# Kernel tuning notes

Hardware: AMD Instinct MI355X
Metric: run time of the kernel (lower is better)

## Reference

```python
import jax, jax.numpy as jnp
import numpy as np

# Hypernetwork config (matches init_kwargs)
INP = 4096      # inp_size
MSK = 64        # mask_size
HID = 64        # node_hidden_size (target-net hidden)
OUT = 10        # out_size (target outputs)
L1, L2, L3 = 64, 256, 128  # hypernet trunk layers
B = 16384       # batch
WVEC = MSK * HID + HID + HID * OUT + OUT  # 4810 generated weights per sample


def _linear_params(key, fan_in, fan_out):
    # torch.nn.Linear default init: U(-1/sqrt(fan_in), 1/sqrt(fan_in))
    lim = 1.0 / np.sqrt(fan_in)
    kw, kb = jax.random.split(key)
    W = jax.random.uniform(kw, (fan_out, fan_in), minval=-lim, maxval=lim, dtype=jnp.float32)
    b = jax.random.uniform(kb, (fan_out,), minval=-lim, maxval=lim, dtype=jnp.float32)
    return W, b


def setup_inputs() -> dict:
    key = jax.random.key(0)
    ks = jax.random.split(key, 6)
    W1, b1 = _linear_params(ks[0], INP, L1)
    W2, b2 = _linear_params(ks[1], L1, L2)
    W3, b3 = _linear_params(ks[2], L2, L3)
    W4, b4 = _linear_params(ks[3], L3, WVEC)
    data = jax.random.normal(ks[4], (B, INP), dtype=jnp.float32)
    mask_idx = jnp.sort(jax.random.randint(ks[5], (B, MSK), 0, INP), axis=1)  # int indices of active features
    return dict(data=data, mask_idx=mask_idx,
                W1=W1, b1=b1, W2=W2, b2=b2, W3=W3, b3=b3, W4=W4, b4=b4)


def reference(data, mask_idx, W1, b1, W2, b2, W3, b3, W4, b4):
    b = data.shape[0]
    # Rebuild the float binary mask [B, INP] from indices (scatter ones)
    rows = jnp.arange(b)[:, None]
    mask = jnp.zeros((b, INP), dtype=data.dtype).at[rows, mask_idx].set(1.0)

    # craft_network: 4-layer MLP on the mask (dropout is identity in eval / for reference)
    h = jax.nn.relu(mask @ W1.T + b1)
    h = jax.nn.relu(h @ W2.T + b2)
    h = jax.nn.relu(h @ W3.T + b3)
    w = h @ W4.T + b4  # [B, WVEC] generated weights per sample

    # Split per-sample generated weights (same layout as InsertableNet)
    iw_end = MSK * HID
    ib_end = iw_end + HID
    ow_end = ib_end + HID * OUT
    inp_w = w[:, :iw_end].reshape(b, HID, MSK)       # [B, H, M]
    inp_b = w[:, iw_end:ib_end]                      # [B, H]
    out_w = w[:, ib_end:ow_end].reshape(b, OUT, HID) # [B, O, H]
    out_b = w[:, ow_end:]                            # [B, O]

    # Per-sample gather of masked features: data[i, mask[i]] -> [B, M]
    xm = jnp.take_along_axis(data, mask_idx, axis=1)

    # Batched tiny 2-layer MLP (replaces the per-sample Python loop)
    hid = jax.nn.relu(jnp.einsum('bhm,bm->bh', inp_w, xm) + inp_b)
    res = jnp.einsum('boh,bh->bo', out_w, hid) + out_b  # [B, OUT]
    return res
```

## Files before the change

kernel.cpp:

```cpp
#include <hip/hip_runtime.h>


typedef _Float16 f16;
typedef _Float16 f16x8 __attribute__((ext_vector_type(8)));
typedef _Float16 f16x4 __attribute__((ext_vector_type(4)));
typedef float    f32x4 __attribute__((ext_vector_type(4)));

#define NPAD 4864

#define BAR() do { asm volatile("s_waitcnt lgkmcnt(0)" ::: "memory"); \
                   __builtin_amdgcn_s_barrier();                      \
                   asm volatile("" ::: "memory"); } while (0)

__global__ __launch_bounds__(256) void k_prep(
    const float* __restrict__ W1, const float* __restrict__ W2,
    const float* __restrict__ W3, const float* __restrict__ W4,
    f16* __restrict__ W1Th, f16* __restrict__ W2h,
    f16* __restrict__ W3h, f16* __restrict__ W4s)
{
    const int tid = blockIdx.x * 256 + threadIdx.x;
    const int stride = gridDim.x * 256;
    for (int e = tid; e < 4096 * 64; e += stride) {
        int j = e >> 6, i = e & 63;
        W1Th[e] = (f16)W1[(size_t)i * 4096 + j];
    }
    for (int e = tid; e < NPAD * 128; e += stride) {
        const int j    = e & 7;
        const int lane = (e >> 3) & 63;
        const int mt   = (e >> 9) & 3;
        const int kk   = (e >> 11) & 3;
        const int c    = e >> 13;
        const int lr = lane & 15, g = lane >> 4;
        const int row = 64 * c + 16 * mt + lr;
        const int col = 32 * kk + 8 * g + j;
        W4s[e] = (row < 4810) ? (f16)W4[(size_t)row * 128 + col] : (f16)0.f;
    }
    for (int e = tid; e < 256 * 64; e += stride)  W2h[e] = (f16)W2[e];
    for (int e = tid; e < 128 * 256; e += stride) W3h[e] = (f16)W3[e];
}

__global__ __launch_bounds__(512, 2) void k_main(
    const float* __restrict__ data, const int* __restrict__ midx,
    const f16* __restrict__ W1Th, const float* __restrict__ b1,
    const f16* __restrict__ W2h, const float* __restrict__ b2,
    const f16* __restrict__ W3h, const float* __restrict__ b3,
    const f16* __restrict__ W4s, const float* __restrict__ b4,
    float* __restrict__ out)
{
    __shared__ __align__(16) int   idx_s[64 * 64];
    __shared__ __align__(16) char  h1b[8192];
    __shared__ __align__(16) char  h2b[32768];
    __shared__ __align__(16) char  h3b[16384];
    __shared__ __align__(16) float xm_s[64 * 68];
    __shared__ __align__(16) float hid_s[64 * 68];
    __shared__ __align__(16) f16   w64_s[64 * 64];
    __shared__ __align__(16) float res_s[64 * 12];
    __shared__ __align__(16) float res_b[64 * 12];

    const int t = threadIdx.x, w = t >> 6, lane = t & 63;
    const int lr = lane & 15, g = lane >> 4;
    const int row0 = blockIdx.x * 64;
    const f32x4 zero = {0.f, 0.f, 0.f, 0.f};

    for (int e = t; e < 4096; e += 512)
        idx_s[e] = midx[(size_t)row0 * 64 + e];
    BAR();

    float xr[64];

    if (w == 7) {
        #pragma unroll
        for (int k = 0; k < 64; ++k)
            xr[k] = data[(size_t)(row0 + k) * 4096 + idx_s[k * 64 + lane]];
        __builtin_amdgcn_sched_barrier(0);
    } else {
        const f32x4 b1v = *(const f32x4*)&b1[lr * 4];
        for (int sp = w; sp < 32; sp += 7) {
            const int s0 = 2 * sp, s1 = s0 + 1;
            f32x4 a0 = zero, a1 = zero;
            #pragma unroll
            for (int tt = 0; tt < 16; ++tt) {
                const int i = g * 16 + tt;
                const int c0 = idx_s[s0 * 64 + i];
                const int q0 = (i > 0) ? idx_s[s0 * 64 + i - 1] : -1;
                const int c1 = idx_s[s1 * 64 + i];
                const int q1 = (i > 0) ? idx_s[s1 * 64 + i - 1] : -1;
                const f16x4 w0 = *(const f16x4*)&W1Th[c0 * 64 + lr * 4];
                const f16x4 w1 = *(const f16x4*)&W1Th[c1 * 64 + lr * 4];
                #pragma unroll
                for (int q = 0; q < 4; ++q) {
                    a0[q] += (c0 != q0) ? (float)w0[q] : 0.f;
                    a1[q] += (c1 != q1) ? (float)w1[q] : 0.f;
                }
            }
            #pragma unroll
            for (int q = 0; q < 4; ++q) {
                a0[q] += __shfl_xor(a0[q], 16);
                a0[q] += __shfl_xor(a0[q], 32);
                a1[q] += __shfl_xor(a1[q], 16);
                a1[q] += __shfl_xor(a1[q], 32);
            }
            if (g == 0) {
                f16x4 h0, h1v;
                #pragma unroll
                for (int q = 0; q < 4; ++q) {
                    h0[q]  = (f16)fmaxf(a0[q] + b1v[q], 0.f);
                    h1v[q] = (f16)fmaxf(a1[q] + b1v[q], 0.f);
                }
                *(f16x4*)(h1b + ((s0 * 128 + lr * 8) ^ ((s0 & 7) << 4))) = h0;
                *(f16x4*)(h1b + ((s1 * 128 + lr * 8) ^ ((s1 & 7) << 4))) = h1v;
            }
        }
    }
    BAR();

    if (w < 7) {
        f16x8 bh[4][2];
        #pragma unroll
        for (int rt = 0; rt < 4; ++rt)
            #pragma unroll
            for (int kk = 0; kk < 2; ++kk) {
                const int s = 16 * rt + lr;
                bh[rt][kk] = *(const f16x8*)(h1b + ((s * 128 + (32 * kk + 8 * g) * 2) ^ ((s & 7) << 4)));
            }
        for (int nb = w; nb < 8; nb += 7) {
            const int n0 = 32 * nb;
            f16x8 a2[2][2];
            #pragma unroll
            for (int mt = 0; mt < 2; ++mt)
                #pragma unroll
                for (int kk = 0; kk < 2; ++kk)
                    a2[mt][kk] = *(const f16x8*)&W2h[(n0 + 16 * mt + lr) * 64 + 32 * kk + 8 * g];
            f32x4 acc2[2][4];
            #pragma unroll
            for (int mt = 0; mt < 2; ++mt)
                #pragma unroll
                for (int rt = 0; rt < 4; ++rt) {
                    acc2[mt][rt] = __builtin_amdgcn_mfma_f32_16x16x32_f16(a2[mt][0], bh[rt][0], zero, 0, 0, 0);
                    acc2[mt][rt] = __builtin_amdgcn_mfma_f32_16x16x32_f16(a2[mt][1], bh[rt][1], acc2[mt][rt], 0, 0, 0);
                }
            #pragma unroll
            for (int mt = 0; mt < 2; ++mt) {
                const f32x4 bv = *(const f32x4*)&b2[n0 + 16 * mt + 4 * g];
                #pragma unroll
                for (int rt = 0; rt < 4; ++rt) {
                    const int s = 16 * rt + lr;
                    f16x4 hv;
                    #pragma unroll
                    for (int q = 0; q < 4; ++q)
                        hv[q] = (f16)fmaxf(acc2[mt][rt][q] + bv[q], 0.f);
                    *(f16x4*)(h2b + ((s * 512 + (n0 + 16 * mt + 4 * g) * 2) ^ ((s & 7) << 4))) = hv;
                }
            }
        }
    }
    BAR();

    if (w < 7) {
        for (int nb = w; nb < 8; nb += 7) {
            const int n0 = 16 * nb;
            f32x4 acc3[4] = {zero, zero, zero, zero};
            #pragma unroll 2
            for (int kk = 0; kk < 8; ++kk) {
                const f16x8 a3 = *(const f16x8*)&W3h[(n0 + lr) * 256 + 32 * kk + 8 * g];
                #pragma unroll
                for (int rt = 0; rt < 4; ++rt) {
                    const int s = 16 * rt + lr;
                    const f16x8 bb = *(const f16x8*)(h2b + ((s * 512 + (32 * kk + 8 * g) * 2) ^ ((s & 7) << 4)));
                    acc3[rt] = __builtin_amdgcn_mfma_f32_16x16x32_f16(a3, bb, acc3[rt], 0, 0, 0);
                }
            }
            const f32x4 bv3 = *(const f32x4*)&b3[n0 + 4 * g];
            #pragma unroll
            for (int rt = 0; rt < 4; ++rt) {
                const int s = 16 * rt + lr;
                f16x4 hv;
                #pragma unroll
                for (int q = 0; q < 4; ++q)
                    hv[q] = (f16)fmaxf(acc3[rt][q] + bv3[q], 0.f);
                *(f16x4*)(h3b + ((s * 256 + (n0 + 4 * g) * 2) ^ ((s & 7) << 4))) = hv;
            }
        }
    }
    BAR();

    f16x8 bfrag[4][4];
    #pragma unroll
    for (int u = 0; u < 4; ++u)
        #pragma unroll
        for (int kk = 0; kk < 4; ++kk) {
            const int s = 16 * u + lr;
            bfrag[kk][u] = *(const f16x8*)(h3b + ((s * 256 + (32 * kk + 8 * g) * 2) ^ ((s & 7) << 4)));
        }
    if (w == 7) {
        #pragma unroll
        for (int k = 0; k < 64; ++k)
            xm_s[k * 68 + lane] = xr[k];
    }
    BAR();

    f16x4 xmr[4][4];
    #pragma unroll
    for (int mt = 0; mt < 4; ++mt)
        #pragma unroll
        for (int u = 0; u < 4; ++u) {
            const f32x4 xv = *(const f32x4*)&xm_s[(16 * u + lr) * 68 + 16 * mt + 4 * g];
            f16x4 xh;
            #pragma unroll
            for (int q = 0; q < 4; ++q) xh[q] = (f16)xv[q];
            xmr[mt][u] = xh;
        }

    const char* W4b = (const char*)W4s;
    const int afoff = lane * 16;

#define LDAF(dst, c, kk) { const char* cb_ = W4b + (size_t)(c) * 16384 + (kk) * 4096 + afoff; \
    dst[0] = *(const f16x8*)(cb_);        dst[1] = *(const f16x8*)(cb_ + 1024); \
    dst[2] = *(const f16x8*)(cb_ + 2048); dst[3] = *(const f16x8*)(cb_ + 3072); }

#define MFMA16(af, kk) { \
    _Pragma("unroll") for (int mt = 0; mt < 4; ++mt) \
    _Pragma("unroll") for (int u = 0; u < 4; ++u) \
        acc[mt][u] = __builtin_amdgcn_mfma_f32_16x16x32_f16(af[mt], bfrag[kk][u], acc[mt][u], 0, 0, 0); }

    for (int c = w; c < 65; c += 8) {
        f16x8 afA[4], afB[4];
        LDAF(afA, c, 0)
        LDAF(afB, c, 1)
        f32x4 acc[4][4];
        #pragma unroll
        for (int mt = 0; mt < 4; ++mt)
            #pragma unroll
            for (int u = 0; u < 4; ++u)
                acc[mt][u] = __builtin_amdgcn_mfma_f32_16x16x32_f16(afA[mt], bfrag[0][u], zero, 0, 0, 0);
        LDAF(afA, c, 2)
        MFMA16(afB, 1)
        LDAF(afB, c, 3)
        MFMA16(afA, 2)
        MFMA16(afB, 3)

        f32x4 bv[4];
        #pragma unroll
        for (int mt = 0; mt < 4; ++mt)
            bv[mt] = *(const f32x4*)&b4[64 * c + 16 * mt + 4 * g];

        if (c < 64) {
            #pragma unroll
            for (int u = 0; u < 4; ++u) {
                float sum = 0.f;
                #pragma unroll
                for (int mt = 0; mt < 4; ++mt)
                    #pragma unroll
                    for (int q = 0; q < 4; ++q)
                        sum += (acc[mt][u][q] + bv[mt][q]) * (float)xmr[mt][u][q];
                sum += __shfl_xor(sum, 16);
                sum += __shfl_xor(sum, 32);
                if (g == 0) hid_s[(16 * u + lr) * 68 + c] = sum;
            }
        } else {
            #pragma unroll
            for (int u = 0; u < 4; ++u)
                #pragma unroll
                for (int mt = 0; mt < 4; ++mt) {
                    f16x4 wv;
                    #pragma unroll
                    for (int q = 0; q < 4; ++q)
                        wv[q] = (f16)(acc[mt][u][q] + bv[mt][q]);
                    *(f16x4*)&w64_s[(16 * u + lr) * 64 + 16 * mt + 4 * g] = wv;
                }
        }
    }
    BAR();

    f16x4 hidr[4][4];
    #pragma unroll
    for (int mt = 0; mt < 4; ++mt)
        #pragma unroll
        for (int u = 0; u < 4; ++u) {
            const int s = 16 * u + lr;
            f16x4 xh;
            #pragma unroll
            for (int q = 0; q < 4; ++q) {
                const int h = 16 * mt + 4 * g + q;
                xh[q] = (f16)fmaxf(hid_s[s * 68 + h] + (float)w64_s[s * 64 + h], 0.f);
            }
            hidr[mt][u] = xh;
        }

    auto do_out = [&](int c) {
        f32x4 bv[4];
        #pragma unroll
        for (int mt = 0; mt < 4; ++mt)
            bv[mt] = *(const f32x4*)&b4[64 * c + 16 * mt + 4 * g];
        f16x8 afA[4], afB[4];
        LDAF(afA, c, 0)
        LDAF(afB, c, 1)
        f32x4 acc[4][4];
        #pragma unroll
        for (int mt = 0; mt < 4; ++mt)
            #pragma unroll
            for (int u = 0; u < 4; ++u)
                acc[mt][u] = __builtin_amdgcn_mfma_f32_16x16x32_f16(afA[mt], bfrag[0][u], zero, 0, 0, 0);
        LDAF(afA, c, 2)
        MFMA16(afB, 1)
        LDAF(afB, c, 3)
        MFMA16(afA, 2)
        MFMA16(afB, 3)
        #pragma unroll
        for (int u = 0; u < 4; ++u) {
            float sum = 0.f;
            #pragma unroll
            for (int mt = 0; mt < 4; ++mt)
                #pragma unroll
                for (int q = 0; q < 4; ++q)
                    sum += (acc[mt][u][q] + bv[mt][q]) * (float)hidr[mt][u][q];
            sum += __shfl_xor(sum, 16);
            sum += __shfl_xor(sum, 32);
            if (g == 0) res_s[(16 * u + lr) * 12 + (c - 65)] = sum;
        }
    };
    do_out(65 + w);
    if (w < 2) do_out(73 + w);

    if (w == 2) {
        f32x4 accb[4] = {zero, zero, zero, zero};
        #pragma unroll
        for (int kk = 0; kk < 4; ++kk) {
            const f16x8 af = *(const f16x8*)(W4b + (size_t)75 * 16384 + kk * 4096 + afoff);
            #pragma unroll
            for (int u = 0; u < 4; ++u)
                accb[u] = __builtin_amdgcn_mfma_f32_16x16x32_f16(af, bfrag[kk][u], accb[u], 0, 0, 0);
        }
        #pragma unroll
        for (int u = 0; u < 4; ++u)
            #pragma unroll
            for (int q = 0; q < 4; ++q) {
                const int o = 4 * g + q;
                if (o < 10)
                    res_b[(16 * u + lr) * 12 + o] = accb[u][q] + b4[4800 + o];
            }
    }
    BAR();

    for (int e = t; e < 640; e += 512)
        out[(size_t)row0 * 10 + e] =
            res_s[(e / 10) * 12 + (e % 10)] + res_b[(e / 10) * 12 + (e % 10)];
#undef LDAF
#undef MFMA16
}

extern "C" void kernel_launch(void* const* d_in, const int* in_sizes, int n_in,
                              void* d_out, int out_size, void* d_ws, size_t ws_size,
                              hipStream_t stream)
{
    const float* data = (const float*)d_in[0];
    const int*   midx = (const int*)d_in[1];
    const float* W1   = (const float*)d_in[2];
    const float* b1   = (const float*)d_in[3];
    const float* W2   = (const float*)d_in[4];
    const float* b2   = (const float*)d_in[5];
    const float* W3   = (const float*)d_in[6];
    const float* b3   = (const float*)d_in[7];
    const float* W4   = (const float*)d_in[8];
    const float* b4   = (const float*)d_in[9];
    float* out = (float*)d_out;

    f16* W1Th = (f16*)d_ws;
    f16* W4s  = W1Th + (size_t)4096 * 64;
    f16* W2h  = W4s + (size_t)NPAD * 128;
    f16* W3h  = W2h + 256 * 64;

    k_prep<<<512, 256, 0, stream>>>(W1, W2, W3, W4, W1Th, W2h, W3h, W4s);
    k_main<<<256, 512, 0, stream>>>(data, midx, W1Th, b1, W2h, b2, W3h, b3,
                                    W4s, b4, out);
}
```

Before: 74.89 us.

## Split gather across two waves and tile W1 transpose through shared memory

In the main kernel, the per-sample data gather moves from one wave handling 64 rows to two waves handling 32 rows each. This halves the register array each gathering wave holds and spreads the gather latency across two waves. In exchange, only six waves remain for the layer-1/2/3 compute, so each compute wave takes on more iterations. The prep kernel also transposes W1 through a padded shared-memory tile, giving coalesced reads and writes in place of strided reads, though it assumes the grid has more than 64 blocks.

```diff
diff --git a/kernel.cpp b/kernel.cpp
--- a/kernel.cpp
+++ b/kernel.cpp
@@ -18,12 +18,28 @@
     f16* __restrict__ W1Th, f16* __restrict__ W2h,
     f16* __restrict__ W3h, f16* __restrict__ W4s)
 {
-    const int tid = blockIdx.x * 256 + threadIdx.x;
-    const int stride = gridDim.x * 256;
-    for (int e = tid; e < 4096 * 64; e += stride) {
-        int j = e >> 6, i = e & 63;
-        W1Th[e] = (f16)W1[(size_t)i * 4096 + j];
-    }
+    const int bid = blockIdx.x;
+    const int t = threadIdx.x;
+
+    if (bid < 64) {
+        __shared__ float tile[64][65];
+        const int r4 = t >> 6, c0 = t & 63;
+        #pragma unroll
+        for (int rr = 0; rr < 16; ++rr) {
+            const int i = rr * 4 + r4;
+            tile[i][c0] = W1[(size_t)i * 4096 + bid * 64 + c0];
+        }
+        __syncthreads();
+        #pragma unroll
+        for (int rr = 0; rr < 16; ++rr) {
+            const int jj = rr * 4 + r4;
+            W1Th[(size_t)(bid * 64 + jj) * 64 + c0] = (f16)tile[c0][jj];
+        }
+        return;
+    }
+
+    const int tid = (bid - 64) * 256 + t;
+    const int stride = (gridDim.x - 64) * 256;
     for (int e = tid; e < NPAD * 128; e += stride) {
         const int j    = e & 7;
         const int lane = (e >> 3) & 63;
@@ -66,16 +82,17 @@
         idx_s[e] = midx[(size_t)row0 * 64 + e];
     BAR();
 
-    float xr[64];
-
-    if (w == 7) {
-        #pragma unroll
-        for (int k = 0; k < 64; ++k)
-            xr[k] = data[(size_t)(row0 + k) * 4096 + idx_s[k * 64 + lane]];
+    float xr[32];
+
+    if (w >= 6) {
+        const int base = (w - 6) * 32;
+        #pragma unroll
+        for (int k = 0; k < 32; ++k)
+            xr[k] = data[(size_t)(row0 + base + k) * 4096 + idx_s[(base + k) * 64 + lane]];
         __builtin_amdgcn_sched_barrier(0);
     } else {
         const f32x4 b1v = *(const f32x4*)&b1[lr * 4];
-        for (int sp = w; sp < 32; sp += 7) {
+        for (int sp = w; sp < 32; sp += 6) {
             const int s0 = 2 * sp, s1 = s0 + 1;
             f32x4 a0 = zero, a1 = zero;
             #pragma unroll
@@ -114,7 +131,7 @@
     }
     BAR();
 
-    if (w < 7) {
+    if (w < 6) {
         f16x8 bh[4][2];
         #pragma unroll
         for (int rt = 0; rt < 4; ++rt)
@@ -123,7 +140,7 @@
                 const int s = 16 * rt + lr;
                 bh[rt][kk] = *(const f16x8*)(h1b + ((s * 128 + (32 * kk + 8 * g) * 2) ^ ((s & 7) << 4)));
             }
-        for (int nb = w; nb < 8; nb += 7) {
+        for (int nb = w; nb < 8; nb += 6) {
             const int n0 = 32 * nb;
             f16x8 a2[2][2];
             #pragma unroll
@@ -156,8 +173,8 @@
     }
     BAR();
 
-    if (w < 7) {
-        for (int nb = w; nb < 8; nb += 7) {
+    if (w < 6) {
+        for (int nb = w; nb < 8; nb += 6) {
             const int n0 = 16 * nb;
             f32x4 acc3[4] = {zero, zero, zero, zero};
             #pragma unroll 2
@@ -192,10 +209,11 @@
             const int s = 16 * u + lr;
             bfrag[kk][u] = *(const f16x8*)(h3b + ((s * 256 + (32 * kk + 8 * g) * 2) ^ ((s & 7) << 4)));
         }
-    if (w == 7) {
-        #pragma unroll
-        for (int k = 0; k < 64; ++k)
-            xm_s[k * 68 + lane] = xr[k];
+    if (w >= 6) {
+        const int base = (w - 6) * 32;
+        #pragma unroll
+        for (int k = 0; k < 32; ++k)
+            xm_s[(base + k) * 68 + lane] = xr[k];
     }
     BAR();
 
```

Measured after the change: 75.26 us. About the same (+0.5%).

## Fuse weight-prep into main kernel with grid-wide atomic barrier

Applied to the files above, without the earlier changes.

Merges the separate weight conversion kernel into the main kernel. Each block's gather wave loads its data rows while the other waves convert weights: the first 64 blocks transpose W1 through shared memory, and the rest convert W4, W2 and W3. A global atomic counter then acts as a grid barrier before the compute phase. This removes one kernel launch and its serialization and overlaps weight prep with the gather, but it relies on all 256 blocks being co-resident and adds a memset plus spin-wait cost.

```diff
diff --git a/kernel.cpp b/kernel.cpp
--- a/kernel.cpp
+++ b/kernel.cpp
@@ -12,39 +12,15 @@
                    __builtin_amdgcn_s_barrier();                      \
                    asm volatile("" ::: "memory"); } while (0)
 
-__global__ __launch_bounds__(256) void k_prep(
-    const float* __restrict__ W1, const float* __restrict__ W2,
-    const float* __restrict__ W3, const float* __restrict__ W4,
+__global__ __launch_bounds__(512, 2) void k_all(
+    const float* __restrict__ data, const int* __restrict__ midx,
+    const float* __restrict__ W1, const float* __restrict__ b1,
+    const float* __restrict__ W2, const float* __restrict__ b2,
+    const float* __restrict__ W3, const float* __restrict__ b3,
+    const float* __restrict__ W4, const float* __restrict__ b4,
     f16* __restrict__ W1Th, f16* __restrict__ W2h,
-    f16* __restrict__ W3h, f16* __restrict__ W4s)
-{
-    const int tid = blockIdx.x * 256 + threadIdx.x;
-    const int stride = gridDim.x * 256;
-    for (int e = tid; e < 4096 * 64; e += stride) {
-        int j = e >> 6, i = e & 63;
-        W1Th[e] = (f16)W1[(size_t)i * 4096 + j];
-    }
-    for (int e = tid; e < NPAD * 128; e += stride) {
-        const int j    = e & 7;
-        const int lane = (e >> 3) & 63;
-        const int mt   = (e >> 9) & 3;
-        const int kk   = (e >> 11) & 3;
-        const int c    = e >> 13;
-        const int lr = lane & 15, g = lane >> 4;
-        const int row = 64 * c + 16 * mt + lr;
-        const int col = 32 * kk + 8 * g + j;
-        W4s[e] = (row < 4810) ? (f16)W4[(size_t)row * 128 + col] : (f16)0.f;
-    }
-    for (int e = tid; e < 256 * 64; e += stride)  W2h[e] = (f16)W2[e];
-    for (int e = tid; e < 128 * 256; e += stride) W3h[e] = (f16)W3[e];
-}
-
-__global__ __launch_bounds__(512, 2) void k_main(
-    const float* __restrict__ data, const int* __restrict__ midx,
-    const f16* __restrict__ W1Th, const float* __restrict__ b1,
-    const f16* __restrict__ W2h, const float* __restrict__ b2,
-    const f16* __restrict__ W3h, const float* __restrict__ b3,
-    const f16* __restrict__ W4s, const float* __restrict__ b4,
+    f16* __restrict__ W3h, f16* __restrict__ W4s,
+    int* __restrict__ sync_cnt,
     float* __restrict__ out)
 {
     __shared__ __align__(16) int   idx_s[64 * 64];
@@ -59,7 +35,8 @@
 
     const int t = threadIdx.x, w = t >> 6, lane = t & 63;
     const int lr = lane & 15, g = lane >> 4;
-    const int row0 = blockIdx.x * 64;
+    const int bid = blockIdx.x;
+    const int row0 = bid * 64;
     const f32x4 zero = {0.f, 0.f, 0.f, 0.f};
 
     for (int e = t; e < 4096; e += 512)
@@ -74,6 +51,61 @@
             xr[k] = data[(size_t)(row0 + k) * 4096 + idx_s[k * 64 + lane]];
         __builtin_amdgcn_sched_barrier(0);
     } else {
+        if (bid < 64) {
+            if (w < 4) {
+                float* tile = (float*)h2b;
+                const int r4 = t >> 6, c0 = t & 63;
+                #pragma unroll
+                for (int rr = 0; rr < 16; ++rr) {
+                    const int i = rr * 4 + r4;
+                    tile[i * 65 + c0] = W1[(size_t)i * 4096 + bid * 64 + c0];
+                }
+            }
+        } else {
+            const int tid = (bid - 64) * 384 + t;
+            const int stride = 192 * 384;
+            if (t < 384) {
+                for (int e = tid; e < NPAD * 128; e += stride) {
+                    const int j    = e & 7;
+                    const int ln   = (e >> 3) & 63;
+                    const int mt   = (e >> 9) & 3;
+                    const int kk   = (e >> 11) & 3;
+                    const int c    = e >> 13;
+                    const int lrr = ln & 15, gg = ln >> 4;
+                    const int row = 64 * c + 16 * mt + lrr;
+                    const int col = 32 * kk + 8 * gg + j;
+                    W4s[e] = (row < 4810) ? (f16)W4[(size_t)row * 128 + col] : (f16)0.f;
+                }
+                for (int e = tid; e < 256 * 64; e += stride)  W2h[e] = (f16)W2[e];
+                for (int e = tid; e < 128 * 256; e += stride) W3h[e] = (f16)W3[e];
+            }
+        }
+    }
+    BAR();
+
+    if (w < 7 && bid < 64 && w < 4) {
+        const float* tile = (const float*)h2b;
+        const int r4 = t >> 6, c0 = t & 63;
+        #pragma unroll
+        for (int rr = 0; rr < 16; ++rr) {
+            const int jj = rr * 4 + r4;
+            W1Th[(size_t)(bid * 64 + jj) * 64 + c0] = (f16)tile[c0 * 65 + jj];
+        }
+    }
+    if (w < 7) asm volatile("s_waitcnt vmcnt(0)" ::: "memory");
+    BAR();
+
+    if (t == 0) {
+        __threadfence();
+        atomicAdd(sync_cnt, 1);
+        while (__hip_atomic_load(sync_cnt, __ATOMIC_ACQUIRE,
+                                 __HIP_MEMORY_SCOPE_AGENT) < 256)
+            __builtin_amdgcn_s_sleep(2);
+        __threadfence();
+    }
+    BAR();
+
+    if (w < 7) {
         const f32x4 b1v = *(const f32x4*)&b1[lr * 4];
         for (int sp = w; sp < 32; sp += 7) {
             const int s0 = 2 * sp, s1 = s0 + 1;
@@ -369,8 +401,9 @@
     f16* W4s  = W1Th + (size_t)4096 * 64;
     f16* W2h  = W4s + (size_t)NPAD * 128;
     f16* W3h  = W2h + 256 * 64;
-
-    k_prep<<<512, 256, 0, stream>>>(W1, W2, W3, W4, W1Th, W2h, W3h, W4s);
-    k_main<<<256, 512, 0, stream>>>(data, midx, W1Th, b1, W2h, b2, W3h, b3,
-                                    W4s, b4, out);
+    int* sync_cnt = (int*)(W3h + 128 * 256);
+
+    hipMemsetAsync(sync_cnt, 0, sizeof(int), stream);
+    k_all<<<256, 512, 0, stream>>>(data, midx, W1, b1, W2, b2, W3, b3, W4, b4,
+                                   W1Th, W2h, W3h, W4s, sync_cnt, out);
 }
```

New measurement: 108.1 us. 1.44x slower.
